# Kernel tuning notes

Measured on AMD Instinct MI355X. Metric: run time of the kernel, lower is better.

Reference implementation:

```python
import jax, jax.numpy as jnp
import numpy as np

N = 50000
E = 800000
D = 128   # input_dim
O = 128   # output_dim


def setup_inputs() -> dict:
    key = jax.random.key(0)
    ks = jax.random.split(key, 12)
    s = 0.05
    inp = {
        "x": jax.random.normal(ks[0], (N, D), dtype=jnp.float32),
        "edge_index": jax.random.randint(ks[1], (2, E), 0, N, dtype=jnp.int64),
        # lin_src_to_dst / lin_dst_to_src
        "w_s2d": jax.random.normal(ks[2], (D, O), dtype=jnp.float32) * s,
        "b_s2d": jnp.zeros((O,), dtype=jnp.float32),
        "w_d2s": jax.random.normal(ks[3], (D, O), dtype=jnp.float32) * s,
        "b_d2s": jnp.zeros((O,), dtype=jnp.float32),
        # edge_mlp: Linear(2D -> D), ReLU, Linear(D -> 1)
        "w_e1": jax.random.normal(ks[4], (2 * D, D), dtype=jnp.float32) * s,
        "b_e1": jnp.zeros((D,), dtype=jnp.float32),
        "w_e2": jax.random.normal(ks[5], (D, 1), dtype=jnp.float32) * s,
        "b_e2": jnp.zeros((1,), dtype=jnp.float32),
        # gate_mlp: Linear(2O -> O), ReLU, Linear(O -> 1)
        "w_g1": jax.random.normal(ks[6], (2 * O, O), dtype=jnp.float32) * s,
        "b_g1": jnp.zeros((O,), dtype=jnp.float32),
        "w_g2": jax.random.normal(ks[7], (O, 1), dtype=jnp.float32) * s,
        "b_g2": jnp.zeros((1,), dtype=jnp.float32),
    }
    return inp


def reference(x, edge_index, w_s2d, b_s2d, w_d2s, b_d2s,
              w_e1, b_e1, w_e2, b_e2, w_g1, b_g1, w_g2, b_g2):
    num_nodes = x.shape[0]
    src = edge_index[0]
    dst = edge_index[1]

    x_src = x[src]                      # [E, D]
    x_dst = x[dst]                      # [E, D]

    # edge-wise contribution score a_ij in (0,1)
    edge_input = jnp.concatenate([x_src, x_dst], axis=-1)          # [E, 2D]
    h_e = jax.nn.relu(edge_input @ w_e1 + b_e1)                    # [E, D]
    edge_score = jax.nn.sigmoid((h_e @ w_e2 + b_e2)[:, 0])         # [E]

    # directional messages, scaled by edge score
    msg_in = (x_src @ w_s2d + b_s2d) * edge_score[:, None]         # [E, O]
    msg_out = (x_dst @ w_d2s + b_d2s) * edge_score[:, None]        # [E, O]

    # scatter-add to nodes
    h_in = jax.ops.segment_sum(msg_in, dst, num_segments=num_nodes)   # [N, O]
    h_out = jax.ops.segment_sum(msg_out, src, num_segments=num_nodes) # [N, O]

    # degree normalization (clamped at 1)
    ones = jnp.ones((src.shape[0],), dtype=x.dtype)
    in_deg = jnp.maximum(jax.ops.segment_sum(ones, dst, num_segments=num_nodes), 1.0)
    out_deg = jnp.maximum(jax.ops.segment_sum(ones, src, num_segments=num_nodes), 1.0)
    h_in = h_in / in_deg[:, None]
    h_out = h_out / out_deg[:, None]

    # node-wise gate fusing the two directions
    gate_input = jnp.concatenate([h_in, h_out], axis=-1)           # [N, 2O]
    h_g = jax.nn.relu(gate_input @ w_g1 + b_g1)                    # [N, O]
    g = jax.nn.sigmoid(h_g @ w_g2 + b_g2)                          # [N, 1]

    fused = g * h_in + (1.0 - g) * h_out                           # [N, O]
    # input_dim == output_dim -> residual is Identity
    return fused + x
```

## Files before the change

kernel.cpp:

```cpp
#include <hip/hip_runtime.h>

#define N_NODES 50000
#define N_EDGES 800000
#define NBKT 391
#define BKT 128
#define MAXREC 2560
#define EPB 4096
#define XCBLK 6250
#define CNTBLK 196

typedef unsigned int u32;
typedef unsigned short u16;
typedef __attribute__((ext_vector_type(2))) float float2v;
typedef __attribute__((ext_vector_type(8))) short bf16x8;
typedef __attribute__((ext_vector_type(4))) float f32x4;

__device__ __forceinline__ float bf_lo(u32 v){ return __uint_as_float(v << 16); }
__device__ __forceinline__ float bf_hi(u32 v){ return __uint_as_float(v & 0xffff0000u); }
__device__ __forceinline__ u16 f2bf(float f){
    u32 u = __float_as_uint(f);
    u += 0x7fffu + ((u >> 16) & 1u);
    return (u16)(u >> 16);
}

#if __has_builtin(__builtin_amdgcn_cvt_pk_f32_fp8) && __has_builtin(__builtin_amdgcn_cvt_pk_fp8_f32)
#define HW_FP8 1
#else
#define HW_FP8 0
#endif

__device__ __forceinline__ u32 enc1_e4m3(float f){
    u32 u = __float_as_uint(f);
    u32 s = (u >> 24) & 0x80u;
    u32 a = u & 0x7fffffffu;
    if (a >= 0x43e00000u) return s | 0x7eu;
    if (a < 0x3c800000u){
        float af = __uint_as_float(a) * 512.f;
        u32 m = (u32)(af + 0.5f);
        return s | m;
    }
    int e = (int)(a >> 23) - 127;
    u32 mant = (a >> 20) & 7u;
    u32 rnd = (a >> 19) & 1u;
    u32 sticky = (a & 0x7ffffu) ? 1u : 0u;
    u32 code = ((u32)(e + 7) << 3) | mant;
    code += (rnd & (sticky | (mant & 1u)));
    if (code > 0x7eu) code = 0x7eu;
    return s | code;
}

template<bool HI>
__device__ __forceinline__ float2v dec2_word(u32 v){
#if HW_FP8
    return __builtin_amdgcn_cvt_pk_f32_fp8(v, HI);
#else
    u32 v16 = HI ? (v >> 16) : (v & 0xffffu);
    float2v r;
    #pragma unroll
    for (int t = 0; t < 2; t++){
        u32 b = (v16 >> (8 * t)) & 0xffu;
        u32 e = (b >> 3) & 15u, m = b & 7u;
        float fv = e ? __uint_as_float(((e + 120u) << 23) | (m << 20)) : (float)m * 0.001953125f;
        r[t] = (b & 0x80u) ? -fv : fv;
    }
    return r;
#endif
}
__device__ __forceinline__ u32 encpk_lo(float a, float b, u32 old){
#if HW_FP8
    return (u32)__builtin_amdgcn_cvt_pk_fp8_f32(a, b, (int)old, false);
#else
    return (old & 0xffff0000u) | enc1_e4m3(a) | (enc1_e4m3(b) << 8);
#endif
}
__device__ __forceinline__ u32 encpk_hi(float a, float b, u32 old){
#if HW_FP8
    return (u32)__builtin_amdgcn_cvt_pk_fp8_f32(a, b, (int)old, true);
#else
    return (old & 0x0000ffffu) | (enc1_e4m3(a) << 16) | (enc1_e4m3(b) << 24);
#endif
}

__global__ __launch_bounds__(256) void setup_kernel(const float* __restrict__ x,
        const float* __restrict__ w_s2d, const float* __restrict__ w_d2s,
        const float* __restrict__ w_e1, const float* __restrict__ w_g1,
        const float* __restrict__ b_e1, const int* __restrict__ eidx,
        uint2* __restrict__ xb2, u32* __restrict__ xf8,
        u16* __restrict__ pk1, u16* __restrict__ pkM,
        u16* __restrict__ pkG, float* __restrict__ bias1, u32* __restrict__ bcnt){
    const int blk = blockIdx.x, tid = threadIdx.x;
    if (blk < XCBLK){
        int i = blk * 256 + tid;
        float4 v = ((const float4*)x)[i];
        uint2 o;
        o.x = (u32)f2bf(v.x) | ((u32)f2bf(v.y) << 16);
        o.y = (u32)f2bf(v.z) | ((u32)f2bf(v.w) << 16);
        xb2[i] = o;
        u32 w8 = encpk_lo(v.x, v.y, 0u);
        xf8[i] = encpk_hi(v.z, v.w, w8);
    } else if (blk < XCBLK + 386){
        int idx = (blk - XCBLK) * 256 + tid;
        if (idx < 32768){
            int j = idx & 7, g = (idx >> 3) & 3, ch = (idx >> 5) & 255, ks = idx >> 13;
            int k = ks * 32 + g * 8 + j;
            float v = (ch < 128) ? w_e1[k * 128 + ch] : w_e1[(128 + k) * 128 + (ch - 128)];
            pk1[idx] = f2bf(v);
        } else if (idx < 65536){
            int i2 = idx - 32768;
            int j = i2 & 7, g = (i2 >> 3) & 3, ch = (i2 >> 5) & 255, ks = i2 >> 13;
            int k = ks * 32 + g * 8 + j;
            float v = (ch < 128) ? w_s2d[k * 128 + ch] : w_d2s[k * 128 + (ch - 128)];
            pkM[i2] = f2bf(v);
        } else if (idx < 98304){
            int i2 = idx - 65536;
            int j = i2 & 7, g = (i2 >> 3) & 3, oc = (i2 >> 5) & 127, ks = i2 >> 12;
            int k = ks * 32 + g * 8 + j;
            pkG[i2] = f2bf(w_g1[k * 128 + oc]);
        } else if (idx < 98560){
            int o = idx - 98304;
            bias1[o] = (o < 128) ? b_e1[o] : 0.f;
        }
    } else {
        __shared__ u32 h[2 * NBKT];
        for (int i = tid; i < 2 * NBKT; i += 256) h[i] = 0u;
        __syncthreads();
        const int e0 = (blk - XCBLK - 386) * EPB;
        for (int i = tid; i < EPB; i += 256){
            int e = e0 + i;
            if (e < N_EDGES){
                atomicAdd(&h[eidx[N_EDGES + e] >> 7], 1u);
                atomicAdd(&h[NBKT + (eidx[e] >> 7)], 1u);
            }
        }
        __syncthreads();
        for (int i = tid; i < 2 * NBKT; i += 256){
            u32 v = h[i];
            if (v) atomicAdd(&bcnt[i], v);
        }
    }
}

__global__ __launch_bounds__(256) void proj_mfma_kernel(const u16* __restrict__ xb16,
        const u16* __restrict__ pk1, const float* __restrict__ bias1, u32* __restrict__ T1){
    const int tid = threadIdx.x;
    const int w = tid >> 6, l = tid & 63;
    const int l16 = l & 15, lg = l >> 4;
    const int n0 = blockIdx.x * 16;
    const int node = n0 + l16;
    bf16x8 bx[4];
    #pragma unroll
    for (int ks = 0; ks < 4; ks++)
        bx[ks] = *(const bf16x8*)(xb16 + node * 128 + ks * 32 + lg * 8);
    #pragma unroll
    for (int ct = 0; ct < 4; ct++){
        const int ch0 = w * 64 + ct * 16;
        f32x4 acc = {0.f, 0.f, 0.f, 0.f};
        #pragma unroll
        for (int ks = 0; ks < 4; ks++){
            bf16x8 a = *(const bf16x8*)(pk1 + ((ks * 256 + ch0 + l16) * 4 + lg) * 8);
            acc = __builtin_amdgcn_mfma_f32_16x16x32_bf16(a, bx[ks], acc, 0, 0, 0);
        }
        const int chb = ch0 + lg * 4;
        float f0 = acc[0] + bias1[chb],     f1 = acc[1] + bias1[chb + 1];
        float f2 = acc[2] + bias1[chb + 2], f3 = acc[3] + bias1[chb + 3];
        u32 wd = encpk_lo(f0, f1, 0u);
        wd = encpk_hi(f2, f3, wd);
        T1[node * 64 + (chb >> 2)] = wd;
    }
}

__global__ __launch_bounds__(256) void edge_score_kernel(const u32* __restrict__ T1w, const int* __restrict__ eidx,
        const float* __restrict__ w_e2, const float* __restrict__ b_e2,
        u16* __restrict__ score){
    const int l16 = threadIdx.x & 15;
    const int e = blockIdx.x * 16 + (threadIdx.x >> 4);
    const int src = eidx[e];
    const int dst = eidx[N_EDGES + e];
    const uint2 a8 = *(const uint2*)(T1w + src * 64 + l16 * 2);
    const uint2 b8 = *(const uint2*)(T1w + dst * 64 + 32 + l16 * 2);
    const float2v* wv = (const float2v*)(w_e2 + l16 * 8);
    const float2v zero = {0.f, 0.f};
    float2v acc = {0.f, 0.f};
    {
        float2v t0 = dec2_word<false>(a8.x) + dec2_word<false>(b8.x);
        float2v t1 = dec2_word<true>(a8.x)  + dec2_word<true>(b8.x);
        float2v t2 = dec2_word<false>(a8.y) + dec2_word<false>(b8.y);
        float2v t3 = dec2_word<true>(a8.y)  + dec2_word<true>(b8.y);
        t0 = __builtin_elementwise_max(t0, zero);
        t1 = __builtin_elementwise_max(t1, zero);
        t2 = __builtin_elementwise_max(t2, zero);
        t3 = __builtin_elementwise_max(t3, zero);
        acc += t0 * wv[0];
        acc += t1 * wv[1];
        acc += t2 * wv[2];
        acc += t3 * wv[3];
    }
    float p = acc[0] + acc[1];
    p += __shfl_xor(p, 1, 64);
    p += __shfl_xor(p, 2, 64);
    p += __shfl_xor(p, 4, 64);
    p += __shfl_xor(p, 8, 64);
    if (l16 == 0){
        float sc = 1.f / (1.f + __expf(-(p + b_e2[0])));
        score[e] = f2bf(sc);
    }
}

__global__ __launch_bounds__(512) void bucket_scan_kernel(const u32* __restrict__ bcnt,
        u32* __restrict__ bbase, u32* __restrict__ bnext){
    __shared__ u32 sa[512], sb[512];
    const int t = threadIdx.x;
    const u32* c = bcnt + blockIdx.x * NBKT;
    u32* base = bbase + blockIdx.x * (NBKT + 1);
    u32* nxt  = bnext + blockIdx.x * NBKT;
    sa[t] = (t < NBKT) ? c[t] : 0u;
    __syncthreads();
    u32 *a = sa, *b = sb;
    for (int off = 1; off < 512; off <<= 1){
        u32 v = a[t]; if (t >= off) v += a[t - off];
        b[t] = v; __syncthreads();
        u32* tmp = a; a = b; b = tmp;
    }
    if (t < NBKT){
        u32 ex = t ? a[t - 1] : 0u;
        base[t] = ex; nxt[t] = ex;
        if (t == NBKT - 1) base[NBKT] = a[t];
    }
}

__global__ __launch_bounds__(256) void bucket1_kernel(const int* __restrict__ eidx, const u16* __restrict__ score,
        u32* __restrict__ bnext, uint2* __restrict__ Bd, uint2* __restrict__ Bs){
    __shared__ u32 hd[NBKT], hs[NBKT];
    __shared__ u32 rbd[NBKT], rbs[NBKT];
    __shared__ u32 ld[NBKT], ls[NBKT];
    const int tid = threadIdx.x;
    for (int i = tid; i < NBKT; i += 256){ hd[i] = 0u; hs[i] = 0u; ld[i] = 0u; ls[i] = 0u; }
    __syncthreads();
    const int e0 = blockIdx.x * EPB;
    for (int i = tid; i < EPB; i += 256){
        int e = e0 + i;
        if (e < N_EDGES){
            atomicAdd(&hd[eidx[N_EDGES + e] >> 7], 1u);
            atomicAdd(&hs[eidx[e] >> 7], 1u);
        }
    }
    __syncthreads();
    for (int i = tid; i < NBKT; i += 256){
        rbd[i] = hd[i] ? atomicAdd(&bnext[i], hd[i]) : 0u;
        rbs[i] = hs[i] ? atomicAdd(&bnext[NBKT + i], hs[i]) : 0u;
    }
    __syncthreads();
    for (int i = tid; i < EPB; i += 256){
        int e = e0 + i;
        if (e < N_EDGES){
            int src = eidx[e], dst = eidx[N_EDGES + e];
            u32 sc = (u32)score[e] << 16;
            int bd = dst >> 7;
            u32 r = atomicAdd(&ld[bd], 1u);
            Bd[rbd[bd] + r] = make_uint2(sc | (u32)src, (u32)(dst & 127));
            int bs_ = src >> 7;
            u32 r2 = atomicAdd(&ls[bs_], 1u);
            Bs[rbs[bs_] + r2] = make_uint2(sc | (u32)dst, (u32)(src & 127));
        }
    }
}

__global__ __launch_bounds__(256) void bucket2_kernel(const uint2* __restrict__ Bd, const uint2* __restrict__ Bs,
        const u32* __restrict__ bbase,
        u32* __restrict__ cnt_dst, u32* __restrict__ start_dst,
        u32* __restrict__ cnt_src, u32* __restrict__ start_src,
        u32* __restrict__ in_pay, u32* __restrict__ out_pay){
    __shared__ u32 pays[MAXREC];
    __shared__ u16 locs[MAXREC];
    __shared__ u32 hist[BKT], nxt[BKT], pref[BKT];
    const int tid = threadIdx.x;
    const int side = blockIdx.x >= NBKT ? 1 : 0;
    const int b = side ? blockIdx.x - NBKT : blockIdx.x;
    const uint2* __restrict__ B = side ? Bs : Bd;
    const u32* bb = bbase + side * (NBKT + 1);
    const u32 base = bb[b];
    const u32 nrec = bb[b + 1] - base;
    u32* cnto = side ? cnt_src : cnt_dst;
    u32* sto  = side ? start_src : start_dst;
    u32* payo = side ? out_pay : in_pay;
    for (int i = tid; i < BKT; i += 256) hist[i] = 0u;
    __syncthreads();
    for (u32 i = tid; i < nrec; i += 256){
        uint2 r = B[base + i];
        if (i < MAXREC){ pays[i] = r.x; locs[i] = (u16)r.y; }
        atomicAdd(&hist[r.y & (BKT - 1)], 1u);
    }
    __syncthreads();
    if (tid < BKT) pref[tid] = hist[tid];
    __syncthreads();
    for (int off = 1; off < BKT; off <<= 1){
        u32 v = 0;
        if (tid < BKT){ v = pref[tid]; if (tid >= off) v += pref[tid - off]; }
        __syncthreads();
        if (tid < BKT) pref[tid] = v;
        __syncthreads();
    }
    if (tid < BKT){
        u32 ex = tid ? pref[tid - 1] : 0u;
        u32 gstart = base + ex;
        nxt[tid] = gstart;
        int node = b * BKT + tid;
        if (node < N_NODES){ cnto[node] = hist[tid]; sto[node] = gstart; }
    }
    __syncthreads();
    for (u32 i = tid; i < nrec; i += 256){
        u32 pay; int loc;
        if (i < MAXREC){ pay = pays[i]; loc = locs[i]; }
        else { uint2 r = B[base + i]; pay = r.x; loc = (int)(r.y & (BKT - 1)); }
        u32 pos = atomicAdd(&nxt[loc], 1u);
        payo[pos] = pay;
    }
}

__global__ __launch_bounds__(256) void gather_kernel(const u32* __restrict__ xf8,
        const u32* __restrict__ in_pay, const u32* __restrict__ out_pay,
        const u32* __restrict__ cnt_dst, const u32* __restrict__ start_dst,
        const u32* __restrict__ cnt_src, const u32* __restrict__ start_src,
        u32* __restrict__ Y, float* __restrict__ ssin, float* __restrict__ ssout){
    const int w = threadIdx.x >> 6, lane = threadIdx.x & 63;
    const int node = blockIdx.x * 2 + (w >> 1);
    const int dir = w & 1;
    const u32* __restrict__ pay = dir ? out_pay : in_pay;
    const u32 deg = dir ? cnt_src[node] : cnt_dst[node];
    const u32 st  = dir ? start_src[node] : start_dst[node];
    const int half = lane >> 5, l5 = lane & 31;
    float2v AL = {0.f, 0.f}, AH = {0.f, 0.f};
    float ss = 0.f;
    u32 j = (u32)half;
    for (; j + 6 < deg; j += 8){
        u32 p0 = pay[st+j], p1 = pay[st+j+2], p2 = pay[st+j+4], p3 = pay[st+j+6];
        u32 v0 = xf8[(p0 & 0xffffu)*32 + l5], v1 = xf8[(p1 & 0xffffu)*32 + l5];
        u32 v2 = xf8[(p2 & 0xffffu)*32 + l5], v3 = xf8[(p3 & 0xffffu)*32 + l5];
        float s0 = __uint_as_float(p0 & 0xffff0000u), s1 = __uint_as_float(p1 & 0xffff0000u);
        float s2 = __uint_as_float(p2 & 0xffff0000u), s3 = __uint_as_float(p3 & 0xffff0000u);
        AL += dec2_word<false>(v0) * s0;  AH += dec2_word<true>(v0) * s0;
        AL += dec2_word<false>(v1) * s1;  AH += dec2_word<true>(v1) * s1;
        AL += dec2_word<false>(v2) * s2;  AH += dec2_word<true>(v2) * s2;
        AL += dec2_word<false>(v3) * s3;  AH += dec2_word<true>(v3) * s3;
        ss += s0 + s1 + s2 + s3;
    }
    for (; j < deg; j += 2){
        u32 pl = pay[st + j];
        u32 v = xf8[(pl & 0xffffu)*32 + l5];
        float sc = __uint_as_float(pl & 0xffff0000u);
        AL += dec2_word<false>(v) * sc;
        AH += dec2_word<true>(v) * sc;
        ss += sc;
    }
    float a0 = AL[0], a1 = AL[1], a2 = AH[0], a3 = AH[1];
    a0 += __shfl_xor(a0, 32, 64);
    a1 += __shfl_xor(a1, 32, 64);
    a2 += __shfl_xor(a2, 32, 64);
    a3 += __shfl_xor(a3, 32, 64);
    ss += __shfl_xor(ss, 32, 64);
    if (half == 0){
        uint2 o;
        o.x = (u32)f2bf(a0) | ((u32)f2bf(a1) << 16);
        o.y = (u32)f2bf(a2) | ((u32)f2bf(a3) << 16);
        *(uint2*)(Y + node * 128 + dir * 64 + l5 * 2) = o;
    }
    if (lane == 0){
        if (dir) ssout[node] = ss; else ssin[node] = ss;
    }
}

__global__ __launch_bounds__(256) void finale_mfma_kernel(const u32* __restrict__ Yw,
        const float* __restrict__ x,
        const u16* __restrict__ pkM, const u16* __restrict__ pkG,
        const float* __restrict__ b_s2d, const float* __restrict__ b_d2s,
        const float* __restrict__ ssin, const float* __restrict__ ssout,
        const u32* __restrict__ cnt_dst, const u32* __restrict__ cnt_src,
        const float* __restrict__ b_g1, const float* __restrict__ w_g2, const float* __restrict__ b_g2,
        float* __restrict__ out){
    __shared__ u32 Hsh[16][132];
    __shared__ float part[16][17];
    __shared__ float gl[16];
    const int tid = threadIdx.x;
    const int w = tid >> 6, l = tid & 63;
    const int l16 = l & 15, lg = l >> 4;
    const int n0 = blockIdx.x * 16;
    const int node = n0 + l16;
    const int dir = w >> 1;
    const int cb = (w & 1) * 64;
    const u16* Yh = (const u16*)Yw;
    bf16x8 yf[4];
    #pragma unroll
    for (int ks = 0; ks < 4; ks++)
        yf[ks] = *(const bf16x8*)(Yh + node * 256 + dir * 128 + ks * 32 + lg * 8);
    const float ssv  = dir ? ssout[node] : ssin[node];
    const float dinv = 1.f / fmaxf((float)(dir ? cnt_src[node] : cnt_dst[node]), 1.f);
    const float* bv = dir ? b_d2s : b_s2d;
    #pragma unroll
    for (int ct = 0; ct < 4; ct++){
        const int chl = cb + ct * 16;
        f32x4 acc = {0.f, 0.f, 0.f, 0.f};
        #pragma unroll
        for (int ks = 0; ks < 4; ks++){
            bf16x8 a = *(const bf16x8*)(pkM + ((ks * 256 + dir * 128 + chl + l16) * 4 + lg) * 8);
            acc = __builtin_amdgcn_mfma_f32_16x16x32_bf16(a, yf[ks], acc, 0, 0, 0);
        }
        const int chb = chl + lg * 4;
        float h0 = (acc[0] + ssv * bv[chb])     * dinv;
        float h1 = (acc[1] + ssv * bv[chb + 1]) * dinv;
        float h2 = (acc[2] + ssv * bv[chb + 2]) * dinv;
        float h3 = (acc[3] + ssv * bv[chb + 3]) * dinv;
        const int wi = (dir * 128 + chb) >> 1;
        Hsh[l16][wi]     = (u32)f2bf(h0) | ((u32)f2bf(h1) << 16);
        Hsh[l16][wi + 1] = (u32)f2bf(h2) | ((u32)f2bf(h3) << 16);
    }
    __syncthreads();
    bf16x8 hb[8];
    #pragma unroll
    for (int ks = 0; ks < 8; ks++)
        hb[ks] = *(const bf16x8*)((const u16*)&Hsh[l16][0] + ks * 32 + lg * 8);
    float p = 0.f;
    #pragma unroll
    for (int ct2 = 0; ct2 < 2; ct2++){
        const int oc0 = w * 32 + ct2 * 16;
        f32x4 acc = {0.f, 0.f, 0.f, 0.f};
        #pragma unroll
        for (int ks = 0; ks < 8; ks++){
            bf16x8 a = *(const bf16x8*)(pkG + ((ks * 128 + oc0 + l16) * 4 + lg) * 8);
            acc = __builtin_amdgcn_mfma_f32_16x16x32_bf16(a, hb[ks], acc, 0, 0, 0);
        }
        const int ob = oc0 + lg * 4;
        #pragma unroll
        for (int r = 0; r < 4; r++)
            p += fmaxf(acc[r] + b_g1[ob + r], 0.f) * w_g2[ob + r];
    }
    part[l16][w * 4 + lg] = p;
    __syncthreads();
    if (tid < 16){
        float s = 0.f;
        #pragma unroll
        for (int i = 0; i < 16; i++) s += part[tid][i];
        gl[tid] = 1.f / (1.f + __expf(-(s + b_g2[0])));
    }
    __syncthreads();
    {
        const int nn = tid >> 4, o = (tid & 15) * 8;
        const float gv = gl[nn];
        const int gbase = (n0 + nn) * 128 + o;
        float4 x0 = *(const float4*)(x + gbase);
        float4 x1 = *(const float4*)(x + gbase + 4);
        float r[8];
        #pragma unroll
        for (int t = 0; t < 4; t++){
            u32 hi = Hsh[nn][(o >> 1) + t];
            u32 ho = Hsh[nn][64 + (o >> 1) + t];
            r[2*t]   = gv * bf_lo(hi) + (1.f - gv) * bf_lo(ho);
            r[2*t+1] = gv * bf_hi(hi) + (1.f - gv) * bf_hi(ho);
        }
        *(float4*)(out + gbase)     = make_float4(r[0]+x0.x, r[1]+x0.y, r[2]+x0.z, r[3]+x0.w);
        *(float4*)(out + gbase + 4) = make_float4(r[4]+x1.x, r[5]+x1.y, r[6]+x1.z, r[7]+x1.w);
    }
}

extern "C" void kernel_launch(void* const* d_in, const int* in_sizes, int n_in,
                              void* d_out, int out_size, void* d_ws, size_t ws_size,
                              hipStream_t stream){
    const float* x     = (const float*)d_in[0];
    const int*   ei    = (const int*)d_in[1];
    const float* w_s2d = (const float*)d_in[2];
    const float* b_s2d = (const float*)d_in[3];
    const float* w_d2s = (const float*)d_in[4];
    const float* b_d2s = (const float*)d_in[5];
    const float* w_e1  = (const float*)d_in[6];
    const float* b_e1  = (const float*)d_in[7];
    const float* w_e2  = (const float*)d_in[8];
    const float* b_e2  = (const float*)d_in[9];
    const float* w_g1  = (const float*)d_in[10];
    const float* b_g1  = (const float*)d_in[11];
    const float* w_g2  = (const float*)d_in[12];
    const float* b_g2  = (const float*)d_in[13];
    float* out = (float*)d_out;
    u32*   T1  = (u32*)d_out;
    uint2* Bd  = (uint2*)d_out;
    uint2* Bs  = Bd + N_EDGES;
    u32*   Y   = (u32*)d_out;

    char* ws = (char*)d_ws;
    size_t off = 0;
    #define TAKE(name, bytes) char* name = ws + off; off += (((size_t)(bytes)) + 511) & ~(size_t)511;
    TAKE(pk1_b,   32768 * 2)
    TAKE(pkM_b,   32768 * 2)
    TAKE(pkG_b,   32768 * 2)
    TAKE(bias1_b, 256 * 4)
    TAKE(xb_b,    (size_t)N_NODES * 128 * 2)
    TAKE(xf8_b,   (size_t)N_NODES * 128)
    TAKE(score_b, (size_t)N_EDGES * 2)
    TAKE(bcnt_b,  (size_t)2 * NBKT * 4)
    TAKE(bbase_b, (size_t)2 * (NBKT + 1) * 4)
    TAKE(bnext_b, (size_t)2 * NBKT * 4)
    TAKE(cnt_b,   (size_t)2 * N_NODES * 4)
    TAKE(sd_b,    (size_t)N_NODES * 4)
    TAKE(ss2_b,   (size_t)N_NODES * 4)
    TAKE(ipay_b,  (size_t)N_EDGES * 4)
    TAKE(opay_b,  (size_t)N_EDGES * 4)
    TAKE(ssin_b,  (size_t)N_NODES * 4)
    TAKE(ssout_b, (size_t)N_NODES * 4)
    #undef TAKE
    (void)ws_size; (void)in_sizes; (void)n_in; (void)out_size;

    hipMemsetAsync(bcnt_b, 0, (size_t)2 * NBKT * 4, stream);
    setup_kernel<<<XCBLK + 386 + CNTBLK, 256, 0, stream>>>(x, w_s2d, w_d2s, w_e1, w_g1, b_e1, ei,
        (uint2*)xb_b, (u32*)xf8_b, (u16*)pk1_b, (u16*)pkM_b, (u16*)pkG_b,
        (float*)bias1_b, (u32*)bcnt_b);
    proj_mfma_kernel<<<N_NODES / 16, 256, 0, stream>>>((const u16*)xb_b,
        (const u16*)pk1_b, (const float*)bias1_b, T1);
    edge_score_kernel<<<N_EDGES / 16, 256, 0, stream>>>((const u32*)T1, ei, w_e2, b_e2,
        (u16*)score_b);
    bucket_scan_kernel<<<2, 512, 0, stream>>>((const u32*)bcnt_b, (u32*)bbase_b, (u32*)bnext_b);
    bucket1_kernel<<<(N_EDGES + EPB - 1) / EPB, 256, 0, stream>>>(ei, (const u16*)score_b,
        (u32*)bnext_b, Bd, Bs);
    bucket2_kernel<<<2 * NBKT, 256, 0, stream>>>(Bd, Bs, (const u32*)bbase_b,
        (u32*)cnt_b, (u32*)sd_b, (u32*)cnt_b + N_NODES, (u32*)ss2_b,
        (u32*)ipay_b, (u32*)opay_b);
    gather_kernel<<<N_NODES / 2, 256, 0, stream>>>((const u32*)xf8_b,
        (const u32*)ipay_b, (const u32*)opay_b,
        (const u32*)cnt_b, (const u32*)sd_b, (const u32*)cnt_b + N_NODES, (const u32*)ss2_b,
        Y, (float*)ssin_b, (float*)ssout_b);
    finale_mfma_kernel<<<N_NODES / 16, 256, 0, stream>>>((const u32*)Y, x,
        (const u16*)pkM_b, (const u16*)pkG_b, b_s2d, b_d2s,
        (const float*)ssin_b, (const float*)ssout_b,
        (const u32*)cnt_b, (const u32*)cnt_b + N_NODES,
        b_g1, w_g2, b_g2, out);
}
```

Measured before the change: 228.8 us.

## Fuse edge scoring into bucketing kernel and unroll gather loop deeper

Removes the standalone edge_score kernel and computes edge scores inside the bucket pass, keeping them in shared memory so the score array no longer round-trips through global memory. Each edge now uses 8 lanes with 16-byte loads instead of 16 lanes with 8-byte loads. The bucket buffers are moved to an offset inside the output so they no longer overlap T1, which the fused kernel reads while writing them. The gather loop also gains a 16-wide unrolled stage for more outstanding loads. The risk is low parallelism: only about 196 blocks now do the score work, so the random T1 gathers may be poorly latency-hidden.

```diff
diff --git a/kernel.cpp b/kernel.cpp
--- a/kernel.cpp
+++ b/kernel.cpp
@@ -169,43 +169,6 @@
     }
 }
 
-__global__ __launch_bounds__(256) void edge_score_kernel(const u32* __restrict__ T1w, const int* __restrict__ eidx,
-        const float* __restrict__ w_e2, const float* __restrict__ b_e2,
-        u16* __restrict__ score){
-    const int l16 = threadIdx.x & 15;
-    const int e = blockIdx.x * 16 + (threadIdx.x >> 4);
-    const int src = eidx[e];
-    const int dst = eidx[N_EDGES + e];
-    const uint2 a8 = *(const uint2*)(T1w + src * 64 + l16 * 2);
-    const uint2 b8 = *(const uint2*)(T1w + dst * 64 + 32 + l16 * 2);
-    const float2v* wv = (const float2v*)(w_e2 + l16 * 8);
-    const float2v zero = {0.f, 0.f};
-    float2v acc = {0.f, 0.f};
-    {
-        float2v t0 = dec2_word<false>(a8.x) + dec2_word<false>(b8.x);
-        float2v t1 = dec2_word<true>(a8.x)  + dec2_word<true>(b8.x);
-        float2v t2 = dec2_word<false>(a8.y) + dec2_word<false>(b8.y);
-        float2v t3 = dec2_word<true>(a8.y)  + dec2_word<true>(b8.y);
-        t0 = __builtin_elementwise_max(t0, zero);
-        t1 = __builtin_elementwise_max(t1, zero);
-        t2 = __builtin_elementwise_max(t2, zero);
-        t3 = __builtin_elementwise_max(t3, zero);
-        acc += t0 * wv[0];
-        acc += t1 * wv[1];
-        acc += t2 * wv[2];
-        acc += t3 * wv[3];
-    }
-    float p = acc[0] + acc[1];
-    p += __shfl_xor(p, 1, 64);
-    p += __shfl_xor(p, 2, 64);
-    p += __shfl_xor(p, 4, 64);
-    p += __shfl_xor(p, 8, 64);
-    if (l16 == 0){
-        float sc = 1.f / (1.f + __expf(-(p + b_e2[0])));
-        score[e] = f2bf(sc);
-    }
-}
-
 __global__ __launch_bounds__(512) void bucket_scan_kernel(const u32* __restrict__ bcnt,
         u32* __restrict__ bbase, u32* __restrict__ bnext){
     __shared__ u32 sa[512], sb[512];
@@ -228,15 +191,53 @@
     }
 }
 
-__global__ __launch_bounds__(256) void bucket1_kernel(const int* __restrict__ eidx, const u16* __restrict__ score,
+__global__ __launch_bounds__(256) void score_bucket_kernel(const u32* __restrict__ T1w,
+        const int* __restrict__ eidx, const float* __restrict__ w_e2, const float* __restrict__ b_e2,
         u32* __restrict__ bnext, uint2* __restrict__ Bd, uint2* __restrict__ Bs){
+    __shared__ u16 ssc[EPB];
     __shared__ u32 hd[NBKT], hs[NBKT];
     __shared__ u32 rbd[NBKT], rbs[NBKT];
     __shared__ u32 ld[NBKT], ls[NBKT];
     const int tid = threadIdx.x;
+    const int e0 = blockIdx.x * EPB;
+    {
+        const float be2 = b_e2[0];
+        const int l8 = tid & 7, esl = tid >> 3;
+        const float2v* wvp = (const float2v*)(w_e2 + l8 * 16);
+        const float2v w0 = wvp[0], w1 = wvp[1], w2 = wvp[2], w3 = wvp[3];
+        const float2v w4 = wvp[4], w5 = wvp[5], w6 = wvp[6], w7 = wvp[7];
+        const float2v zero = {0.f, 0.f};
+        for (int pass = 0; pass < EPB / 32; pass++){
+            const int e = e0 + pass * 32 + esl;
+            float p = 0.f;
+            if (e < N_EDGES){
+                const int src = eidx[e];
+                const int dst = eidx[N_EDGES + e];
+                const uint4 a8 = *(const uint4*)(T1w + src * 64 + l8 * 4);
+                const uint4 b8 = *(const uint4*)(T1w + dst * 64 + 32 + l8 * 4);
+                float2v acc = {0.f, 0.f};
+                float2v t;
+                t = __builtin_elementwise_max(dec2_word<false>(a8.x) + dec2_word<false>(b8.x), zero); acc += t * w0;
+                t = __builtin_elementwise_max(dec2_word<true >(a8.x) + dec2_word<true >(b8.x), zero); acc += t * w1;
+                t = __builtin_elementwise_max(dec2_word<false>(a8.y) + dec2_word<false>(b8.y), zero); acc += t * w2;
+                t = __builtin_elementwise_max(dec2_word<true >(a8.y) + dec2_word<true >(b8.y), zero); acc += t * w3;
+                t = __builtin_elementwise_max(dec2_word<false>(a8.z) + dec2_word<false>(b8.z), zero); acc += t * w4;
+                t = __builtin_elementwise_max(dec2_word<true >(a8.z) + dec2_word<true >(b8.z), zero); acc += t * w5;
+                t = __builtin_elementwise_max(dec2_word<false>(a8.w) + dec2_word<false>(b8.w), zero); acc += t * w6;
+                t = __builtin_elementwise_max(dec2_word<true >(a8.w) + dec2_word<true >(b8.w), zero); acc += t * w7;
+                p = acc[0] + acc[1];
+            }
+            p += __shfl_xor(p, 1, 64);
+            p += __shfl_xor(p, 2, 64);
+            p += __shfl_xor(p, 4, 64);
+            if (l8 == 0 && e < N_EDGES){
+                float sc = 1.f / (1.f + __expf(-(p + be2)));
+                ssc[pass * 32 + esl] = f2bf(sc);
+            }
+        }
+    }
     for (int i = tid; i < NBKT; i += 256){ hd[i] = 0u; hs[i] = 0u; ld[i] = 0u; ls[i] = 0u; }
     __syncthreads();
-    const int e0 = blockIdx.x * EPB;
     for (int i = tid; i < EPB; i += 256){
         int e = e0 + i;
         if (e < N_EDGES){
@@ -254,7 +255,7 @@
         int e = e0 + i;
         if (e < N_EDGES){
             int src = eidx[e], dst = eidx[N_EDGES + e];
-            u32 sc = (u32)score[e] << 16;
+            u32 sc = (u32)ssc[i] << 16;
             int bd = dst >> 7;
             u32 r = atomicAdd(&ld[bd], 1u);
             Bd[rbd[bd] + r] = make_uint2(sc | (u32)src, (u32)(dst & 127));
@@ -332,6 +333,27 @@
     float2v AL = {0.f, 0.f}, AH = {0.f, 0.f};
     float ss = 0.f;
     u32 j = (u32)half;
+    for (; j + 14 < deg; j += 16){
+        u32 p0 = pay[st+j],    p1 = pay[st+j+2],  p2 = pay[st+j+4],  p3 = pay[st+j+6];
+        u32 p4 = pay[st+j+8],  p5 = pay[st+j+10], p6 = pay[st+j+12], p7 = pay[st+j+14];
+        u32 v0 = xf8[(p0 & 0xffffu)*32 + l5], v1 = xf8[(p1 & 0xffffu)*32 + l5];
+        u32 v2 = xf8[(p2 & 0xffffu)*32 + l5], v3 = xf8[(p3 & 0xffffu)*32 + l5];
+        u32 v4 = xf8[(p4 & 0xffffu)*32 + l5], v5 = xf8[(p5 & 0xffffu)*32 + l5];
+        u32 v6 = xf8[(p6 & 0xffffu)*32 + l5], v7 = xf8[(p7 & 0xffffu)*32 + l5];
+        float s0 = __uint_as_float(p0 & 0xffff0000u), s1 = __uint_as_float(p1 & 0xffff0000u);
+        float s2 = __uint_as_float(p2 & 0xffff0000u), s3 = __uint_as_float(p3 & 0xffff0000u);
+        float s4 = __uint_as_float(p4 & 0xffff0000u), s5 = __uint_as_float(p5 & 0xffff0000u);
+        float s6 = __uint_as_float(p6 & 0xffff0000u), s7 = __uint_as_float(p7 & 0xffff0000u);
+        AL += dec2_word<false>(v0) * s0;  AH += dec2_word<true>(v0) * s0;
+        AL += dec2_word<false>(v1) * s1;  AH += dec2_word<true>(v1) * s1;
+        AL += dec2_word<false>(v2) * s2;  AH += dec2_word<true>(v2) * s2;
+        AL += dec2_word<false>(v3) * s3;  AH += dec2_word<true>(v3) * s3;
+        AL += dec2_word<false>(v4) * s4;  AH += dec2_word<true>(v4) * s4;
+        AL += dec2_word<false>(v5) * s5;  AH += dec2_word<true>(v5) * s5;
+        AL += dec2_word<false>(v6) * s6;  AH += dec2_word<true>(v6) * s6;
+        AL += dec2_word<false>(v7) * s7;  AH += dec2_word<true>(v7) * s7;
+        ss += s0 + s1 + s2 + s3 + s4 + s5 + s6 + s7;
+    }
     for (; j + 6 < deg; j += 8){
         u32 p0 = pay[st+j], p1 = pay[st+j+2], p2 = pay[st+j+4], p3 = pay[st+j+6];
         u32 v0 = xf8[(p0 & 0xffffu)*32 + l5], v1 = xf8[(p1 & 0xffffu)*32 + l5];
@@ -480,7 +502,7 @@
     const float* b_g2  = (const float*)d_in[13];
     float* out = (float*)d_out;
     u32*   T1  = (u32*)d_out;
-    uint2* Bd  = (uint2*)d_out;
+    uint2* Bd  = (uint2*)((u32*)d_out + 3200000);
     uint2* Bs  = Bd + N_EDGES;
     u32*   Y   = (u32*)d_out;
 
@@ -493,7 +515,6 @@
     TAKE(bias1_b, 256 * 4)
     TAKE(xb_b,    (size_t)N_NODES * 128 * 2)
     TAKE(xf8_b,   (size_t)N_NODES * 128)
-    TAKE(score_b, (size_t)N_EDGES * 2)
     TAKE(bcnt_b,  (size_t)2 * NBKT * 4)
     TAKE(bbase_b, (size_t)2 * (NBKT + 1) * 4)
     TAKE(bnext_b, (size_t)2 * NBKT * 4)
@@ -513,10 +534,8 @@
         (float*)bias1_b, (u32*)bcnt_b);
     proj_mfma_kernel<<<N_NODES / 16, 256, 0, stream>>>((const u16*)xb_b,
         (const u16*)pk1_b, (const float*)bias1_b, T1);
-    edge_score_kernel<<<N_EDGES / 16, 256, 0, stream>>>((const u32*)T1, ei, w_e2, b_e2,
-        (u16*)score_b);
     bucket_scan_kernel<<<2, 512, 0, stream>>>((const u32*)bcnt_b, (u32*)bbase_b, (u32*)bnext_b);
-    bucket1_kernel<<<(N_EDGES + EPB - 1) / EPB, 256, 0, stream>>>(ei, (const u16*)score_b,
+    score_bucket_kernel<<<(N_EDGES + EPB - 1) / EPB, 256, 0, stream>>>((const u32*)T1, ei, w_e2, b_e2,
         (u32*)bnext_b, Bd, Bs);
     bucket2_kernel<<<2 * NBKT, 256, 0, stream>>>(Bd, Bs, (const u32*)bbase_b,
         (u32*)cnt_b, (u32*)sd_b, (u32*)cnt_b + N_NODES, (u32*)ss2_b,
```

After: 289.8 us. 1.27x slower.
